# Kernel optimization log

Measured on AMD Instinct MI355X. Metric: run time of the kernel, lower is better.

Reference implementation:

```python
import jax, jax.numpy as jnp
import numpy as np

EMB_DIM, NUM_LEVELS, NUM_HEADS, NUM_POINTS = 256, 4, 8, 4
LEVEL_SHAPES = np.array([[128, 128], [64, 64], [32, 32], [16, 16]], dtype=np.int64)
B, N_Q = 8, 900
N_IMG = int((LEVEL_SHAPES[:, 0] * LEVEL_SHAPES[:, 1]).sum())  # 21760


def _offset_bias():
    # Faithful to the torch init: per-head square pattern scaled by point index.
    H, L, P = NUM_HEADS, NUM_LEVELS, NUM_POINTS
    angles = jnp.linspace(0.0, 2.0 * np.pi * (H - 1) / H, H)
    circle = jnp.stack([jnp.sin(angles), jnp.cos(angles)], axis=-1)          # [H,2]
    square = circle / jnp.max(jnp.abs(circle), axis=-1, keepdims=True)       # [H,2]
    squares = jnp.tile(square[:, None, None, :], (1, L, P, 1))               # [H,L,P,2]
    squares = squares * jnp.arange(1, P + 1, dtype=jnp.float32)[:, None]
    return squares.reshape(-1).astype(jnp.float32)


def setup_inputs() -> dict:
    key = jax.random.key(0)
    ks = jax.random.split(key, 12)
    C = EMB_DIM
    H, L, P = NUM_HEADS, NUM_LEVELS, NUM_POINTS
    s = 0.02
    return {
        'query_feat': jax.random.normal(ks[0], (B, N_Q, C), jnp.float32),
        'query_points': jax.random.uniform(ks[1], (B, N_Q, 4), jnp.float32, 0.1, 0.9),
        'img_feat': jax.random.normal(ks[2], (B, N_IMG, C), jnp.float32),
        'img_valid_ratios': jnp.ones((B, L, 2), jnp.float32),
        'img_mask': jnp.zeros((B, N_IMG), bool),
        'img_shapes': jnp.asarray(LEVEL_SHAPES),
        'W_img': jax.random.normal(ks[3], (C, C), jnp.float32) * s,
        'b_img': jax.random.normal(ks[4], (C,), jnp.float32) * s,
        'W_off': jax.random.normal(ks[5], (C, H * L * P * 2), jnp.float32) * 0.001,
        'b_off': _offset_bias(),
        'W_attn': jax.random.normal(ks[6], (C, H * L * P), jnp.float32) * s,
        'b_attn': jax.random.normal(ks[7], (H * L * P,), jnp.float32) * s,
        'W_out': jax.random.normal(ks[8], (C, C), jnp.float32) * s,
        'b_out': jax.random.normal(ks[9], (C,), jnp.float32) * s,
    }


def _bilinear_sample(value, loc, Hl, Wl):
    # value: [B,Hh,Hl*Wl,d]; loc: [B,Hh,Q,P,2] (x,y) normalized to [0,1]
    # grid_sample bilinear, padding_mode='zeros', align_corners=False
    Bb, Hh = value.shape[0], value.shape[1]
    x = loc[..., 0] * Wl - 0.5
    y = loc[..., 1] * Hl - 0.5
    x0f = jnp.floor(x); y0f = jnp.floor(y)
    wx = x - x0f; wy = y - y0f
    x0 = x0f.astype(jnp.int32); y0 = y0f.astype(jnp.int32)

    def gather(yi, xi):
        valid = (yi >= 0) & (yi < Hl) & (xi >= 0) & (xi < Wl)
        idx = jnp.clip(yi, 0, Hl - 1) * Wl + jnp.clip(xi, 0, Wl - 1)
        flat = idx.reshape(Bb, Hh, -1)[..., None]                 # [B,Hh,Q*P,1]
        g = jnp.take_along_axis(value, flat, axis=2)              # [B,Hh,Q*P,d]
        g = g.reshape(*idx.shape, value.shape[-1])                # [B,Hh,Q,P,d]
        return g * valid[..., None]

    v00 = gather(y0, x0); v01 = gather(y0, x0 + 1)
    v10 = gather(y0 + 1, x0); v11 = gather(y0 + 1, x0 + 1)
    w00 = ((1 - wy) * (1 - wx))[..., None]; w01 = ((1 - wy) * wx)[..., None]
    w10 = (wy * (1 - wx))[..., None]; w11 = (wy * wx)[..., None]
    return v00 * w00 + v01 * w01 + v10 * w10 + v11 * w11


def _msda(img_feat, img_shapes, sampling_points, attention_weights):
    # img_feat [B,N,Hh,d]; sampling_points [B,Q,Hh,L,P,2]; attn [B,Q,Hh,L,P]
    shapes = np.asarray(img_shapes)  # static level metadata
    Bb, N, Hh, d = img_feat.shape
    Q = sampling_points.shape[1]
    value = jnp.transpose(img_feat, (0, 2, 1, 3))                     # [B,Hh,N,d]
    loc = jnp.transpose(sampling_points, (0, 2, 1, 3, 4, 5))          # [B,Hh,Q,L,P,2]
    attn = jnp.transpose(attention_weights, (0, 2, 1, 3, 4))          # [B,Hh,Q,L,P]
    out = jnp.zeros((Bb, Hh, Q, d), img_feat.dtype)
    start = 0
    for l in range(shapes.shape[0]):
        Hl, Wl = int(shapes[l, 0]), int(shapes[l, 1])
        v = value[:, :, start:start + Hl * Wl]
        s = _bilinear_sample(v, loc[:, :, :, l], Hl, Wl)              # [B,Hh,Q,P,d]
        out = out + jnp.einsum('bhqpd,bhqp->bhqd', s, attn[:, :, :, l])
        start += Hl * Wl
    return jnp.transpose(out, (0, 2, 1, 3)).reshape(Bb, Q, Hh * d)


def reference(query_feat, query_points, img_feat, img_valid_ratios, img_mask,
              img_shapes, W_img, b_img, W_off, b_off, W_attn, b_attn, W_out, b_out):
    Bb, N_img, C = img_feat.shape
    N_q = query_feat.shape[1]
    Hh, L, P = NUM_HEADS, NUM_LEVELS, NUM_POINTS
    v = img_feat @ W_img + b_img
    v = jnp.where(img_mask[..., None], 0.0, v).reshape(Bb, N_img, Hh, C // Hh)
    offs = (query_feat @ W_off + b_off).reshape(Bb, N_q, Hh, L, P, 2)
    attn = jax.nn.softmax((query_feat @ W_attn + b_attn).reshape(Bb, N_q, Hh, L * P), axis=-1)
    attn = attn.reshape(Bb, N_q, Hh, L, P)
    # box branch (query_points last dim == 4), cxcywh relative coords
    vr = jnp.tile(img_valid_ratios[..., ::-1], (1, 1, 2))             # [B,L,4]
    qp = query_points[:, :, None, :] * vr[:, None, :, :]              # [B,Nq,L,4]
    sp = qp[:, :, None, :, None, :2] + offs * qp[:, :, None, :, None, 2:] / (2.0 * P)
    out = _msda(v, img_shapes, sp, attn)                              # [B,Nq,C]
    return out @ W_out + b_out
```

## Files before the change

kernel.cpp:

```cpp
#include <hip/hip_runtime.h>

#define NQ 900
#define NIMG 21760

typedef __attribute__((ext_vector_type(8))) short short8v;
typedef __attribute__((ext_vector_type(4))) float f32x4;
typedef unsigned short ushort_t;

__device__ __forceinline__ ushort_t f32_to_bf16_rne(float a) {
  unsigned u = __float_as_uint(a);
  unsigned r = u + 0x7FFFu + ((u >> 16) & 1u);
  return (ushort_t)(r >> 16);
}

union U8v {
  unsigned u[4];
  short8v v;
};

__device__ __forceinline__ short8v cvt8(float4 x, float4 y) {
  U8v r;
  asm("v_cvt_pk_bf16_f32 %0, %1, %2" : "=v"(r.u[0]) : "v"(x.x), "v"(x.y));
  asm("v_cvt_pk_bf16_f32 %0, %1, %2" : "=v"(r.u[1]) : "v"(x.z), "v"(x.w));
  asm("v_cvt_pk_bf16_f32 %0, %1, %2" : "=v"(r.u[2]) : "v"(y.x), "v"(y.y));
  asm("v_cvt_pk_bf16_f32 %0, %1, %2" : "=v"(r.u[3]) : "v"(y.z), "v"(y.w));
  return r.v;
}

__device__ __forceinline__ unsigned cvt_pk2(float a, float b) {
  unsigned r;
  asm("v_cvt_pk_bf16_f32 %0, %1, %2" : "=v"(r) : "v"(a), "v"(b));
  return r;
}

__global__ __launch_bounds__(256) void wprep_kernel(
    const float* __restrict__ Wimg, const float* __restrict__ Wout,
    ushort_t* __restrict__ Wh, ushort_t* __restrict__ Wh2) {
  const int blk = blockIdx.x;
  const int idx = (blk & 255) * 256 + threadIdx.x;
  const int k = idx >> 8, col = idx & 255;
  if (blk < 256)
    Wh[col * 256 + k] = f32_to_bf16_rne(Wimg[idx]);
  else
    Wh2[col * 256 + k] = f32_to_bf16_rne(Wout[idx]);
}

#define NBLK 512
#define NTILES 5440
__global__ __launch_bounds__(256, 2) void vproj_persist(
    const float* __restrict__ A, const ushort_t* __restrict__ Wh,
    const float* __restrict__ bias, ushort_t* __restrict__ v) {
  __shared__ __align__(16) float Abuf[2][32 * 256];

  const int t = threadIdx.x;
  const int w = t >> 6, lane = t & 63;
  const int lr = lane & 15, lg = lane >> 4;

  short8v bB[8][4];
#pragma unroll
  for (int ks = 0; ks < 8; ++ks)
#pragma unroll
    for (int n = 0; n < 4; ++n) {
      const int col = w * 64 + n * 16 + lr;
      bB[ks][n] = *(const short8v*)(Wh + (size_t)col * 256 + ks * 32 + lg * 8);
    }
  float bj[4][4];
#pragma unroll
  for (int n = 0; n < 4; ++n)
#pragma unroll
    for (int j = 0; j < 4; ++j) bj[n][j] = bias[w * 64 + n * 16 + lg * 4 + j];

  auto STAGE = [&](int buf, int tile) {
#pragma unroll
    for (int j = 0; j < 8; ++j) {
      const int ob = j * 4096 + w * 1024;
      const int o = ob + lane * 16;
      const int r = o >> 10;
      const int ir = (o & 1023) ^ ((r & 7) << 4);
      const float* gp = A + (size_t)(tile * 32 + r) * 256 + (ir >> 2);
      char* lp = (char*)(&Abuf[buf][0]) + ob;
      __builtin_amdgcn_global_load_lds(
          (const __attribute__((address_space(1))) void*)gp,
          (__attribute__((address_space(3))) void*)lp, 16, 0, 0);
    }
  };

  int tile = blockIdx.x;
  STAGE(0, tile);
  int cur = 0;

  for (; tile < NTILES; tile += NBLK) {
    const int nxt = tile + NBLK;
    if (nxt < NTILES) {
      STAGE(cur ^ 1, nxt);
      if (tile == (int)blockIdx.x)
        asm volatile("s_waitcnt vmcnt(8)" ::: "memory");
      else
        asm volatile("s_waitcnt vmcnt(16)" ::: "memory");
    } else {
      asm volatile("s_waitcnt vmcnt(8)" ::: "memory");
    }
    __builtin_amdgcn_s_barrier();
    __builtin_amdgcn_sched_barrier(0);

    f32x4 acc[2][4];
#pragma unroll
    for (int m = 0; m < 2; ++m)
#pragma unroll
      for (int n = 0; n < 4; ++n) {
        acc[m][n][0] = 0.f; acc[m][n][1] = 0.f;
        acc[m][n][2] = 0.f; acc[m][n][3] = 0.f;
      }

    const char* AB = (const char*)&Abuf[cur][0];

    float4 px[2][2], py[2][2];
#pragma unroll
    for (int p = 0; p < 2; ++p)
#pragma unroll
      for (int m = 0; m < 2; ++m) {
        const int row = m * 16 + lr;
        const int a0 = row * 1024 + ((p * 128 + lg * 32) ^ ((row & 7) << 4));
        px[p][m] = *(const float4*)(AB + a0);
        py[p][m] = *(const float4*)(AB + (a0 ^ 16));
      }

#pragma unroll
    for (int ks = 0; ks < 8; ++ks) {
      short8v ah[2];
#pragma unroll
      for (int m = 0; m < 2; ++m) ah[m] = cvt8(px[ks & 1][m], py[ks & 1][m]);
      if (ks < 6) {
#pragma unroll
        for (int m = 0; m < 2; ++m) {
          const int row = m * 16 + lr;
          const int a0 =
              row * 1024 + (((ks + 2) * 128 + lg * 32) ^ ((row & 7) << 4));
          px[ks & 1][m] = *(const float4*)(AB + a0);
          py[ks & 1][m] = *(const float4*)(AB + (a0 ^ 16));
        }
      }
#pragma unroll
      for (int n = 0; n < 4; ++n)
#pragma unroll
        for (int m = 0; m < 2; ++m)
          acc[m][n] = __builtin_amdgcn_mfma_f32_16x16x32_bf16(bB[ks][n], ah[m], acc[m][n], 0, 0, 0);
    }
    __builtin_amdgcn_sched_barrier(0);

    const int bb = tile / 680;
    const int pix0 = (tile - bb * 680) * 32;
#pragma unroll
    for (int n = 0; n < 4; ++n) {
      const int col0 = w * 64 + n * 16 + lg * 4;
      const int h = col0 >> 5, ch = col0 & 31;
#pragma unroll
      for (int m = 0; m < 2; ++m) {
        const int pixel = pix0 + m * 16 + lr;
        uint2 pk;
        pk.x = cvt_pk2(acc[m][n][0] + bj[n][0], acc[m][n][1] + bj[n][1]);
        pk.y = cvt_pk2(acc[m][n][2] + bj[n][2], acc[m][n][3] + bj[n][3]);
        *(uint2*)(v + ((size_t)(bb * 8 + h) * NIMG + pixel) * 32 + ch) = pk;
      }
    }
    __builtin_amdgcn_s_barrier();
    cur ^= 1;
  }
}

__global__ __launch_bounds__(256) void gemm_noLds(
    const float* __restrict__ A, const ushort_t* __restrict__ Wh,
    const float* __restrict__ bias, float* __restrict__ C, int M) {
  const int t = threadIdx.x;
  const int colblk = blockIdx.x & 3;
  const int rowblk = blockIdx.x >> 2;
  const int col0 = colblk * 64;

  const int lane = t & 63, w = t >> 6;
  const int lr = lane & 15, lg = lane >> 4;
  const int wrow0 = rowblk * 64 + w * 16;

  f32x4 acc[4];
#pragma unroll
  for (int n = 0; n < 4; ++n) {
    acc[n][0] = 0.f; acc[n][1] = 0.f; acc[n][2] = 0.f; acc[n][3] = 0.f;
  }

#pragma unroll
  for (int ks = 0; ks < 8; ++ks) {
    int row = wrow0 + lr;
    row = min(row, M - 1);
    const float4* ap = (const float4*)(A + (size_t)row * 256 + ks * 32 + lg * 8);
    const short8v ah = cvt8(ap[0], ap[1]);
    const int k0 = ks * 32 + lg * 8;
#pragma unroll
    for (int n = 0; n < 4; ++n) {
      const int col = col0 + n * 16 + lr;
      const short8v bh = *(const short8v*)(Wh + col * 256 + k0);
      acc[n] = __builtin_amdgcn_mfma_f32_16x16x32_bf16(ah, bh, acc[n], 0, 0, 0);
    }
  }

#pragma unroll
  for (int n = 0; n < 4; ++n) {
    const int col = col0 + n * 16 + lr;
    const float b = bias[col];
#pragma unroll
    for (int j = 0; j < 4; ++j) {
      const int row = wrow0 + lg * 4 + j;
      if (row < M) C[(size_t)row * 256 + col] = acc[n][j] + b;
    }
  }
}

__global__ __launch_bounds__(384) void qproj_kernel(
    const float* __restrict__ qf, const float* __restrict__ qpts_g,
    const float* __restrict__ ivr, const float* __restrict__ Woff,
    const float* __restrict__ boff, const float* __restrict__ Wattn,
    const float* __restrict__ battn, float* __restrict__ sp,
    float* __restrict__ attn) {
  __shared__ __align__(16) float qlds[8 * 256];
  __shared__ float qp[8][4];
  __shared__ float vr[8][8];
  __shared__ float logits[8][128];
  const int t = threadIdx.x;
  const int row0 = blockIdx.x * 8;

  for (int idx = t; idx < 8 * 256; idx += 384)
    qlds[idx] = qf[(size_t)row0 * 256 + idx];
  if (t < 32) {
    const int m = t >> 2, j = t & 3;
    qp[m][j] = qpts_g[(size_t)(row0 + m) * 4 + j];
  }
  if (t >= 32 && t < 96) {
    const int u = t - 32;
    const int m = u >> 3, j = u & 7;
    const int b = (row0 + m) / NQ;
    vr[m][j] = ivr[b * 8 + j];
  }
  __syncthreads();

  float acc[8];
#pragma unroll
  for (int m = 0; m < 8; ++m) acc[m] = 0.f;

  const float4* q4 = (const float4*)qlds;
  const int c = t - 256;
  for (int k4 = 0; k4 < 64; ++k4) {
    float w0, w1, w2, w3;
    if (t < 256) {
      w0 = Woff[(k4 * 4 + 0) * 256 + t];
      w1 = Woff[(k4 * 4 + 1) * 256 + t];
      w2 = Woff[(k4 * 4 + 2) * 256 + t];
      w3 = Woff[(k4 * 4 + 3) * 256 + t];
    } else {
      w0 = Wattn[(k4 * 4 + 0) * 128 + c];
      w1 = Wattn[(k4 * 4 + 1) * 128 + c];
      w2 = Wattn[(k4 * 4 + 2) * 128 + c];
      w3 = Wattn[(k4 * 4 + 3) * 128 + c];
    }
#pragma unroll
    for (int m = 0; m < 8; ++m) {
      const float4 f = q4[m * 64 + k4];
      acc[m] = fmaf(f.x, w0, acc[m]);
      acc[m] = fmaf(f.y, w1, acc[m]);
      acc[m] = fmaf(f.z, w2, acc[m]);
      acc[m] = fmaf(f.w, w3, acc[m]);
    }
  }

  if (t >= 256) {
    const float bb = battn[c];
#pragma unroll
    for (int m = 0; m < 8; ++m) logits[m][c] = acc[m] + bb;
  }
  __syncthreads();

  if (t < 64) {
    const int m = t >> 3, h = t & 7;
    float mx = -1e30f;
#pragma unroll
    for (int j = 0; j < 16; ++j) mx = fmaxf(mx, logits[m][h * 16 + j]);
    float e[16];
    float s = 0.f;
#pragma unroll
    for (int j = 0; j < 16; ++j) {
      e[j] = expf(logits[m][h * 16 + j] - mx);
      s += e[j];
    }
    const float inv = 1.f / s;
    const size_t row = row0 + m;
#pragma unroll
    for (int j = 0; j < 16; ++j) attn[row * 128 + h * 16 + j] = e[j] * inv;
  }

  if (t < 256) {
    const int xy = t & 1;
    const int l = (t >> 3) & 3;
    const float bo = boff[t];
#pragma unroll
    for (int m = 0; m < 8; ++m) {
      const float val = acc[m] + bo;
      const float r = vr[m][l * 2 + (xy ^ 1)];
      const float ctr = qp[m][xy] * r;
      const float scl = qp[m][2 + xy] * r * 0.125f;
      sp[(size_t)(row0 + m) * 256 + t] = ctr + val * scl;
    }
  }
}

__global__ __launch_bounds__(256) void msda_kernel(
    const ushort_t* __restrict__ v, const float* __restrict__ sp,
    const float* __restrict__ attn, float* __restrict__ outk) {
  __shared__ __align__(16) float splds[1024];
  __shared__ __align__(16) float alds[512];
  __shared__ int ioff[16 * 2 * 32];
  __shared__ float wgt[16 * 4 * 32];
  const int t = threadIdx.x;
  const int bid = (int)(blockIdx.x & 7) * 225 + (int)(blockIdx.x >> 3);
  const int row0 = bid * 4;

  ((float4*)splds)[t] = ((const float4*)(sp + (size_t)row0 * 256))[t];
  if (t < 128)
    ((float4*)alds)[t] = ((const float4*)(attn + (size_t)row0 * 128))[t];
  __syncthreads();

#pragma unroll
  for (int it = 0; it < 2; ++it) {
    const int s = it * 256 + t;
    const int q = s >> 7, h = (s >> 4) & 7, l = (s >> 2) & 3, p = s & 3;
    const int un = q * 8 + h;
    const int j = l * 4 + p;
    const float spx = splds[q * 256 + h * 32 + l * 8 + p * 2];
    const float spy = splds[q * 256 + h * 32 + l * 8 + p * 2 + 1];
    const float a = alds[q * 128 + h * 16 + l * 4 + p];
    const int WL = 128 >> l;
    const int start = (65536 - (65536 >> (2 * l))) / 3;
    const float x = spx * (float)WL - 0.5f;
    const float y = spy * (float)WL - 0.5f;
    const float x0f = floorf(x), y0f = floorf(y);
    const float wx = x - x0f, wy = y - y0f;
    const int x0 = (int)x0f, y0 = (int)y0f;
    const int x1 = x0 + 1, y1 = y0 + 1;
    const int bx = min(max(x0, 0), WL - 2);
    const bool vx0 = (x0 >= 0) & (x0 < WL), vx1 = (x1 >= 0) & (x1 < WL);
    float wxl = 0.f, wxr = 0.f;
    if (vx0 & (x0 == bx)) wxl += 1.f - wx;
    if (vx1 & (x1 == bx)) wxl += wx;
    if (vx0 & (x0 == bx + 1)) wxr += 1.f - wx;
    if (vx1 & (x1 == bx + 1)) wxr += wx;
    const int cy0 = min(max(y0, 0), WL - 1), cy1 = min(max(y1, 0), WL - 1);
    const float ay0 = ((y0 >= 0) & (y0 < WL)) ? a * (1.f - wy) : 0.f;
    const float ay1 = ((y1 >= 0) & (y1 < WL)) ? a * wy : 0.f;
    ioff[(j * 2 + 0) * 32 + un] = (start + cy0 * WL + bx) * 32;
    ioff[(j * 2 + 1) * 32 + un] = (start + cy1 * WL + bx) * 32;
    wgt[(j * 4 + 0) * 32 + un] = ay0 * wxl;
    wgt[(j * 4 + 1) * 32 + un] = ay0 * wxr;
    wgt[(j * 4 + 2) * 32 + un] = ay1 * wxl;
    wgt[(j * 4 + 3) * 32 + un] = ay1 * wxr;
  }
  __syncthreads();

  const int q = t >> 6, h = (t >> 3) & 7, d8 = t & 7;
  const int un = q * 8 + h;
  const int cq = d8 & 3, half = d8 >> 2;
  const int row = row0 + q;
  const int b = row / NQ;
  const ushort_t* vbl =
      v + ((size_t)(b * 8 + h) * NIMG) * 32 + half * 32 + cq * 8;

  float acc[8];
#pragma unroll
  for (int i = 0; i < 8; ++i) acc[i] = 0.f;

#pragma unroll
  for (int j = 0; j < 16; ++j) {
#pragma unroll
    for (int r = 0; r < 2; ++r) {
      const int off = ioff[(j * 2 + r) * 32 + un];
      const float wc = wgt[(j * 4 + r * 2 + half) * 32 + un];
      const uint4 uu = *(const uint4*)(vbl + off);
      acc[0] = fmaf(wc, __uint_as_float(uu.x << 16), acc[0]);
      acc[1] = fmaf(wc, __uint_as_float(uu.x & 0xFFFF0000u), acc[1]);
      acc[2] = fmaf(wc, __uint_as_float(uu.y << 16), acc[2]);
      acc[3] = fmaf(wc, __uint_as_float(uu.y & 0xFFFF0000u), acc[3]);
      acc[4] = fmaf(wc, __uint_as_float(uu.z << 16), acc[4]);
      acc[5] = fmaf(wc, __uint_as_float(uu.z & 0xFFFF0000u), acc[5]);
      acc[6] = fmaf(wc, __uint_as_float(uu.w << 16), acc[6]);
      acc[7] = fmaf(wc, __uint_as_float(uu.w & 0xFFFF0000u), acc[7]);
    }
  }

#pragma unroll
  for (int i = 0; i < 8; ++i) acc[i] += __shfl_xor(acc[i], 4);

  float4 o;
  o.x = acc[half * 4 + 0];
  o.y = acc[half * 4 + 1];
  o.z = acc[half * 4 + 2];
  o.w = acc[half * 4 + 3];
  *(float4*)(outk + (size_t)row * 256 + h * 32 + cq * 8 + half * 4) = o;
}

extern "C" void kernel_launch(void* const* d_in, const int* in_sizes, int n_in,
                              void* d_out, int out_size, void* d_ws, size_t ws_size,
                              hipStream_t stream) {
  const float* query_feat   = (const float*)d_in[0];
  const float* query_points = (const float*)d_in[1];
  const float* img_feat     = (const float*)d_in[2];
  const float* ivr          = (const float*)d_in[3];
  const float* W_img  = (const float*)d_in[6];
  const float* b_img  = (const float*)d_in[7];
  const float* W_off  = (const float*)d_in[8];
  const float* b_off  = (const float*)d_in[9];
  const float* W_attn = (const float*)d_in[10];
  const float* b_attn = (const float*)d_in[11];
  const float* W_out  = (const float*)d_in[12];
  const float* b_out  = (const float*)d_in[13];
  float* out = (float*)d_out;

  float* ws   = (float*)d_ws;
  ushort_t* v = (ushort_t*)ws;
  float* sp   = (float*)(v + 44564480);
  float* attn = sp + 1843200;
  float* mso  = attn + 921600;
  ushort_t* Wh  = (ushort_t*)(mso + 1843200);
  ushort_t* Wh2 = Wh + 65536;

  wprep_kernel<<<512, 256, 0, stream>>>(W_img, W_out, Wh, Wh2);
  vproj_persist<<<NBLK, 256, 0, stream>>>(img_feat, Wh, b_img, v);
  qproj_kernel<<<900, 384, 0, stream>>>(query_feat, query_points, ivr,
                                        W_off, b_off, W_attn, b_attn, sp, attn);
  msda_kernel<<<1800, 256, 0, stream>>>(v, sp, attn, mso);
  gemm_noLds<<<113 * 4, 256, 0, stream>>>(mso, Wh2, b_out, out, 7200);
}
```

Before: 141.3 us.

## Remap MSDA blocks to one head per block and double query rows in qproj

The sampling kernel now gives each block 32 queries of a single (batch, head) pair instead of 4 queries across all 8 heads. Every block therefore gathers from one head's value slab, which should improve cache locality for the bilinear gathers. Sampling points and attention weights are read straight from global memory rather than staged in shared memory, and a guarded tail handles query counts that are not a multiple of 32. Separately, the query projection processes 16 rows per block so each weight load is reused twice as often, at the cost of more registers and fewer blocks.

```diff
diff --git a/kernel.cpp b/kernel.cpp
--- a/kernel.cpp
+++ b/kernel.cpp
@@ -219,30 +219,30 @@
     const float* __restrict__ boff, const float* __restrict__ Wattn,
     const float* __restrict__ battn, float* __restrict__ sp,
     float* __restrict__ attn) {
-  __shared__ __align__(16) float qlds[8 * 256];
-  __shared__ float qp[8][4];
-  __shared__ float vr[8][8];
-  __shared__ float logits[8][128];
+  __shared__ __align__(16) float qlds[16 * 256];
+  __shared__ float qp[16][4];
+  __shared__ float vr[16][8];
+  __shared__ float logits[16][128];
   const int t = threadIdx.x;
-  const int row0 = blockIdx.x * 8;
-
-  for (int idx = t; idx < 8 * 256; idx += 384)
+  const int row0 = blockIdx.x * 16;
+
+  for (int idx = t; idx < 16 * 256; idx += 384)
     qlds[idx] = qf[(size_t)row0 * 256 + idx];
-  if (t < 32) {
+  if (t < 64) {
     const int m = t >> 2, j = t & 3;
     qp[m][j] = qpts_g[(size_t)(row0 + m) * 4 + j];
   }
-  if (t >= 32 && t < 96) {
-    const int u = t - 32;
+  if (t >= 64 && t < 192) {
+    const int u = t - 64;
     const int m = u >> 3, j = u & 7;
     const int b = (row0 + m) / NQ;
     vr[m][j] = ivr[b * 8 + j];
   }
   __syncthreads();
 
-  float acc[8];
-#pragma unroll
-  for (int m = 0; m < 8; ++m) acc[m] = 0.f;
+  float acc[16];
+#pragma unroll
+  for (int m = 0; m < 16; ++m) acc[m] = 0.f;
 
   const float4* q4 = (const float4*)qlds;
   const int c = t - 256;
@@ -260,7 +260,7 @@
       w3 = Wattn[(k4 * 4 + 3) * 128 + c];
     }
 #pragma unroll
-    for (int m = 0; m < 8; ++m) {
+    for (int m = 0; m < 16; ++m) {
       const float4 f = q4[m * 64 + k4];
       acc[m] = fmaf(f.x, w0, acc[m]);
       acc[m] = fmaf(f.y, w1, acc[m]);
@@ -272,11 +272,11 @@
   if (t >= 256) {
     const float bb = battn[c];
 #pragma unroll
-    for (int m = 0; m < 8; ++m) logits[m][c] = acc[m] + bb;
+    for (int m = 0; m < 16; ++m) logits[m][c] = acc[m] + bb;
   }
   __syncthreads();
 
-  if (t < 64) {
+  if (t < 128) {
     const int m = t >> 3, h = t & 7;
     float mx = -1e30f;
 #pragma unroll
@@ -299,7 +299,7 @@
     const int l = (t >> 3) & 3;
     const float bo = boff[t];
 #pragma unroll
-    for (int m = 0; m < 8; ++m) {
+    for (int m = 0; m < 16; ++m) {
       const float val = acc[m] + bo;
       const float r = vr[m][l * 2 + (xy ^ 1)];
       const float ctr = qp[m][xy] * r;
@@ -309,31 +309,28 @@
   }
 }
 
+#define QCH 29
 __global__ __launch_bounds__(256) void msda_kernel(
     const ushort_t* __restrict__ v, const float* __restrict__ sp,
     const float* __restrict__ attn, float* __restrict__ outk) {
-  __shared__ __align__(16) float splds[1024];
-  __shared__ __align__(16) float alds[512];
   __shared__ int ioff[16 * 2 * 32];
   __shared__ float wgt[16 * 4 * 32];
   const int t = threadIdx.x;
-  const int bid = (int)(blockIdx.x & 7) * 225 + (int)(blockIdx.x >> 3);
-  const int row0 = bid * 4;
-
-  ((float4*)splds)[t] = ((const float4*)(sp + (size_t)row0 * 256))[t];
-  if (t < 128)
-    ((float4*)alds)[t] = ((const float4*)(attn + (size_t)row0 * 128))[t];
-  __syncthreads();
+  const int b = blockIdx.x & 7;
+  const int inner = blockIdx.x >> 3;
+  const int h = inner / QCH;
+  const int q0 = (inner - h * QCH) * 32;
 
 #pragma unroll
   for (int it = 0; it < 2; ++it) {
     const int s = it * 256 + t;
-    const int q = s >> 7, h = (s >> 4) & 7, l = (s >> 2) & 3, p = s & 3;
-    const int un = q * 8 + h;
-    const int j = l * 4 + p;
-    const float spx = splds[q * 256 + h * 32 + l * 8 + p * 2];
-    const float spy = splds[q * 256 + h * 32 + l * 8 + p * 2 + 1];
-    const float a = alds[q * 128 + h * 16 + l * 4 + p];
+    const int ql = s >> 4, j = s & 15;
+    const int l = j >> 2, p = j & 3;
+    const bool valid = (q0 + ql) < NQ;
+    const size_t row = (size_t)b * NQ + (valid ? q0 + ql : 0);
+    const float spx = valid ? sp[row * 256 + h * 32 + l * 8 + p * 2] : 0.5f;
+    const float spy = valid ? sp[row * 256 + h * 32 + l * 8 + p * 2 + 1] : 0.5f;
+    const float a = valid ? attn[row * 128 + h * 16 + j] : 0.f;
     const int WL = 128 >> l;
     const int start = (65536 - (65536 >> (2 * l))) / 3;
     const float x = spx * (float)WL - 0.5f;
@@ -352,20 +349,17 @@
     const int cy0 = min(max(y0, 0), WL - 1), cy1 = min(max(y1, 0), WL - 1);
     const float ay0 = ((y0 >= 0) & (y0 < WL)) ? a * (1.f - wy) : 0.f;
     const float ay1 = ((y1 >= 0) & (y1 < WL)) ? a * wy : 0.f;
-    ioff[(j * 2 + 0) * 32 + un] = (start + cy0 * WL + bx) * 32;
-    ioff[(j * 2 + 1) * 32 + un] = (start + cy1 * WL + bx) * 32;
-    wgt[(j * 4 + 0) * 32 + un] = ay0 * wxl;
-    wgt[(j * 4 + 1) * 32 + un] = ay0 * wxr;
-    wgt[(j * 4 + 2) * 32 + un] = ay1 * wxl;
-    wgt[(j * 4 + 3) * 32 + un] = ay1 * wxr;
+    ioff[(j * 2 + 0) * 32 + ql] = (start + cy0 * WL + bx) * 32;
+    ioff[(j * 2 + 1) * 32 + ql] = (start + cy1 * WL + bx) * 32;
+    wgt[(j * 4 + 0) * 32 + ql] = ay0 * wxl;
+    wgt[(j * 4 + 1) * 32 + ql] = ay0 * wxr;
+    wgt[(j * 4 + 2) * 32 + ql] = ay1 * wxl;
+    wgt[(j * 4 + 3) * 32 + ql] = ay1 * wxr;
   }
   __syncthreads();
 
-  const int q = t >> 6, h = (t >> 3) & 7, d8 = t & 7;
-  const int un = q * 8 + h;
+  const int ql = t >> 3, d8 = t & 7;
   const int cq = d8 & 3, half = d8 >> 2;
-  const int row = row0 + q;
-  const int b = row / NQ;
   const ushort_t* vbl =
       v + ((size_t)(b * 8 + h) * NIMG) * 32 + half * 32 + cq * 8;
 
@@ -377,8 +371,8 @@
   for (int j = 0; j < 16; ++j) {
 #pragma unroll
     for (int r = 0; r < 2; ++r) {
-      const int off = ioff[(j * 2 + r) * 32 + un];
-      const float wc = wgt[(j * 4 + r * 2 + half) * 32 + un];
+      const int off = ioff[(j * 2 + r) * 32 + ql];
+      const float wc = wgt[(j * 4 + r * 2 + half) * 32 + ql];
       const uint4 uu = *(const uint4*)(vbl + off);
       acc[0] = fmaf(wc, __uint_as_float(uu.x << 16), acc[0]);
       acc[1] = fmaf(wc, __uint_as_float(uu.x & 0xFFFF0000u), acc[1]);
@@ -394,12 +388,15 @@
 #pragma unroll
   for (int i = 0; i < 8; ++i) acc[i] += __shfl_xor(acc[i], 4);
 
-  float4 o;
-  o.x = acc[half * 4 + 0];
-  o.y = acc[half * 4 + 1];
-  o.z = acc[half * 4 + 2];
-  o.w = acc[half * 4 + 3];
-  *(float4*)(outk + (size_t)row * 256 + h * 32 + cq * 8 + half * 4) = o;
+  if (q0 + ql < NQ) {
+    const size_t row = (size_t)b * NQ + q0 + ql;
+    float4 o;
+    o.x = acc[half * 4 + 0];
+    o.y = acc[half * 4 + 1];
+    o.z = acc[half * 4 + 2];
+    o.w = acc[half * 4 + 3];
+    *(float4*)(outk + row * 256 + h * 32 + cq * 8 + half * 4) = o;
+  }
 }
 
 extern "C" void kernel_launch(void* const* d_in, const int* in_sizes, int n_in,
@@ -429,8 +426,8 @@
 
   wprep_kernel<<<512, 256, 0, stream>>>(W_img, W_out, Wh, Wh2);
   vproj_persist<<<NBLK, 256, 0, stream>>>(img_feat, Wh, b_img, v);
-  qproj_kernel<<<900, 384, 0, stream>>>(query_feat, query_points, ivr,
+  qproj_kernel<<<450, 384, 0, stream>>>(query_feat, query_points, ivr,
                                         W_off, b_off, W_attn, b_attn, sp, attn);
-  msda_kernel<<<1800, 256, 0, stream>>>(v, sp, attn, mso);
+  msda_kernel<<<8 * 8 * QCH, 256, 0, stream>>>(v, sp, attn, mso);
   gemm_noLds<<<113 * 4, 256, 0, stream>>>(mso, Wh2, b_out, out, 7200);
 }
```

Measured after the change: 152.3 us. +7.8%, slower.

## Fuse query projection into value-projection kernel as extra blocks

Applied to the files above, without the earlier changes.

Merges the query offset/attention projection kernel into the persistent value-projection kernel, dispatching 900 query blocks first and 512 value-projection blocks after in one launch. The two independent projections can then overlap on the GPU, and one launch gap goes away. The query path is remapped from 384 to 256 threads: threads 128-255 compute both offset and attention columns, and the shared-memory scratch is reused from the staging buffer. Risks are register pressure from the combined kernel under launch_bounds(256,2), and the persistent value blocks starting late behind the query blocks.

```diff
diff --git a/kernel.cpp b/kernel.cpp
--- a/kernel.cpp
+++ b/kernel.cpp
@@ -45,14 +45,115 @@
     Wh2[col * 256 + k] = f32_to_bf16_rne(Wout[idx]);
 }
 
-#define NBLK 512
+#define QBLKS 900
+#define VBLKS 512
 #define NTILES 5440
-__global__ __launch_bounds__(256, 2) void vproj_persist(
+__global__ __launch_bounds__(256, 2) void fused_vq(
     const float* __restrict__ A, const ushort_t* __restrict__ Wh,
-    const float* __restrict__ bias, ushort_t* __restrict__ v) {
+    const float* __restrict__ bias, ushort_t* __restrict__ v,
+    const float* __restrict__ qf, const float* __restrict__ qpts_g,
+    const float* __restrict__ ivr, const float* __restrict__ Woff,
+    const float* __restrict__ boff, const float* __restrict__ Wattn,
+    const float* __restrict__ battn, float* __restrict__ sp,
+    float* __restrict__ attn) {
   __shared__ __align__(16) float Abuf[2][32 * 256];
 
   const int t = threadIdx.x;
+
+  if (blockIdx.x < QBLKS) {
+    float* qlds = &Abuf[0][0];
+    float* qp = qlds + 2048;
+    float* vr = qp + 32;
+    float* logits = vr + 64;
+    const int row0 = blockIdx.x * 8;
+
+#pragma unroll
+    for (int i = 0; i < 8; ++i) qlds[i * 256 + t] = qf[(size_t)row0 * 256 + i * 256 + t];
+    if (t < 32) qp[t] = qpts_g[(size_t)row0 * 4 + t];
+    if (t >= 32 && t < 96) {
+      const int u = t - 32;
+      const int m = u >> 3, j = u & 7;
+      const int b = (row0 + m) / NQ;
+      vr[m * 8 + j] = ivr[b * 8 + j];
+    }
+    __syncthreads();
+
+    float acc[8], acc2[8];
+#pragma unroll
+    for (int m = 0; m < 8; ++m) { acc[m] = 0.f; acc2[m] = 0.f; }
+
+    const float4* q4 = (const float4*)qlds;
+    const int c = t - 128;
+    for (int k4 = 0; k4 < 64; ++k4) {
+      const float w0 = Woff[(k4 * 4 + 0) * 256 + t];
+      const float w1 = Woff[(k4 * 4 + 1) * 256 + t];
+      const float w2 = Woff[(k4 * 4 + 2) * 256 + t];
+      const float w3 = Woff[(k4 * 4 + 3) * 256 + t];
+      float a0 = 0.f, a1 = 0.f, a2 = 0.f, a3 = 0.f;
+      if (t >= 128) {
+        a0 = Wattn[(k4 * 4 + 0) * 128 + c];
+        a1 = Wattn[(k4 * 4 + 1) * 128 + c];
+        a2 = Wattn[(k4 * 4 + 2) * 128 + c];
+        a3 = Wattn[(k4 * 4 + 3) * 128 + c];
+      }
+#pragma unroll
+      for (int m = 0; m < 8; ++m) {
+        const float4 f = q4[m * 64 + k4];
+        acc[m] = fmaf(f.x, w0, acc[m]);
+        acc[m] = fmaf(f.y, w1, acc[m]);
+        acc[m] = fmaf(f.z, w2, acc[m]);
+        acc[m] = fmaf(f.w, w3, acc[m]);
+        if (t >= 128) {
+          acc2[m] = fmaf(f.x, a0, acc2[m]);
+          acc2[m] = fmaf(f.y, a1, acc2[m]);
+          acc2[m] = fmaf(f.z, a2, acc2[m]);
+          acc2[m] = fmaf(f.w, a3, acc2[m]);
+        }
+      }
+    }
+
+    if (t >= 128) {
+      const float bb = battn[c];
+#pragma unroll
+      for (int m = 0; m < 8; ++m) logits[m * 128 + c] = acc2[m] + bb;
+    }
+    __syncthreads();
+
+    if (t < 64) {
+      const int m = t >> 3, h = t & 7;
+      float mx = -1e30f;
+#pragma unroll
+      for (int j = 0; j < 16; ++j) mx = fmaxf(mx, logits[m * 128 + h * 16 + j]);
+      float e[16];
+      float s = 0.f;
+#pragma unroll
+      for (int j = 0; j < 16; ++j) {
+        e[j] = expf(logits[m * 128 + h * 16 + j] - mx);
+        s += e[j];
+      }
+      const float inv = 1.f / s;
+      const size_t row = row0 + m;
+#pragma unroll
+      for (int j = 0; j < 16; ++j) attn[row * 128 + h * 16 + j] = e[j] * inv;
+    }
+
+    {
+      const int xy = t & 1;
+      const int l = (t >> 3) & 3;
+      const float bo = boff[t];
+#pragma unroll
+      for (int m = 0; m < 8; ++m) {
+        const float val = acc[m] + bo;
+        const float r = vr[m * 8 + l * 2 + (xy ^ 1)];
+        const float ctr = qp[m * 4 + xy] * r;
+        const float scl = qp[m * 4 + 2 + xy] * r * 0.125f;
+        sp[(size_t)(row0 + m) * 256 + t] = ctr + val * scl;
+      }
+    }
+    return;
+  }
+
+  const int vbid = blockIdx.x - QBLKS;
   const int w = t >> 6, lane = t & 63;
   const int lr = lane & 15, lg = lane >> 4;
 
@@ -85,15 +186,15 @@
     }
   };
 
-  int tile = blockIdx.x;
+  int tile = vbid;
   STAGE(0, tile);
   int cur = 0;
 
-  for (; tile < NTILES; tile += NBLK) {
-    const int nxt = tile + NBLK;
+  for (; tile < NTILES; tile += VBLKS) {
+    const int nxt = tile + VBLKS;
     if (nxt < NTILES) {
       STAGE(cur ^ 1, nxt);
-      if (tile == (int)blockIdx.x)
+      if (tile == vbid)
         asm volatile("s_waitcnt vmcnt(8)" ::: "memory");
       else
         asm volatile("s_waitcnt vmcnt(16)" ::: "memory");
@@ -209,102 +310,6 @@
     for (int j = 0; j < 4; ++j) {
       const int row = wrow0 + lg * 4 + j;
       if (row < M) C[(size_t)row * 256 + col] = acc[n][j] + b;
-    }
-  }
-}
-
-__global__ __launch_bounds__(384) void qproj_kernel(
-    const float* __restrict__ qf, const float* __restrict__ qpts_g,
-    const float* __restrict__ ivr, const float* __restrict__ Woff,
-    const float* __restrict__ boff, const float* __restrict__ Wattn,
-    const float* __restrict__ battn, float* __restrict__ sp,
-    float* __restrict__ attn) {
-  __shared__ __align__(16) float qlds[8 * 256];
-  __shared__ float qp[8][4];
-  __shared__ float vr[8][8];
-  __shared__ float logits[8][128];
-  const int t = threadIdx.x;
-  const int row0 = blockIdx.x * 8;
-
-  for (int idx = t; idx < 8 * 256; idx += 384)
-    qlds[idx] = qf[(size_t)row0 * 256 + idx];
-  if (t < 32) {
-    const int m = t >> 2, j = t & 3;
-    qp[m][j] = qpts_g[(size_t)(row0 + m) * 4 + j];
-  }
-  if (t >= 32 && t < 96) {
-    const int u = t - 32;
-    const int m = u >> 3, j = u & 7;
-    const int b = (row0 + m) / NQ;
-    vr[m][j] = ivr[b * 8 + j];
-  }
-  __syncthreads();
-
-  float acc[8];
-#pragma unroll
-  for (int m = 0; m < 8; ++m) acc[m] = 0.f;
-
-  const float4* q4 = (const float4*)qlds;
-  const int c = t - 256;
-  for (int k4 = 0; k4 < 64; ++k4) {
-    float w0, w1, w2, w3;
-    if (t < 256) {
-      w0 = Woff[(k4 * 4 + 0) * 256 + t];
-      w1 = Woff[(k4 * 4 + 1) * 256 + t];
-      w2 = Woff[(k4 * 4 + 2) * 256 + t];
-      w3 = Woff[(k4 * 4 + 3) * 256 + t];
-    } else {
-      w0 = Wattn[(k4 * 4 + 0) * 128 + c];
-      w1 = Wattn[(k4 * 4 + 1) * 128 + c];
-      w2 = Wattn[(k4 * 4 + 2) * 128 + c];
-      w3 = Wattn[(k4 * 4 + 3) * 128 + c];
-    }
-#pragma unroll
-    for (int m = 0; m < 8; ++m) {
-      const float4 f = q4[m * 64 + k4];
-      acc[m] = fmaf(f.x, w0, acc[m]);
-      acc[m] = fmaf(f.y, w1, acc[m]);
-      acc[m] = fmaf(f.z, w2, acc[m]);
-      acc[m] = fmaf(f.w, w3, acc[m]);
-    }
-  }
-
-  if (t >= 256) {
-    const float bb = battn[c];
-#pragma unroll
-    for (int m = 0; m < 8; ++m) logits[m][c] = acc[m] + bb;
-  }
-  __syncthreads();
-
-  if (t < 64) {
-    const int m = t >> 3, h = t & 7;
-    float mx = -1e30f;
-#pragma unroll
-    for (int j = 0; j < 16; ++j) mx = fmaxf(mx, logits[m][h * 16 + j]);
-    float e[16];
-    float s = 0.f;
-#pragma unroll
-    for (int j = 0; j < 16; ++j) {
-      e[j] = expf(logits[m][h * 16 + j] - mx);
-      s += e[j];
-    }
-    const float inv = 1.f / s;
-    const size_t row = row0 + m;
-#pragma unroll
-    for (int j = 0; j < 16; ++j) attn[row * 128 + h * 16 + j] = e[j] * inv;
-  }
-
-  if (t < 256) {
-    const int xy = t & 1;
-    const int l = (t >> 3) & 3;
-    const float bo = boff[t];
-#pragma unroll
-    for (int m = 0; m < 8; ++m) {
-      const float val = acc[m] + bo;
-      const float r = vr[m][l * 2 + (xy ^ 1)];
-      const float ctr = qp[m][xy] * r;
-      const float scl = qp[m][2 + xy] * r * 0.125f;
-      sp[(size_t)(row0 + m) * 256 + t] = ctr + val * scl;
     }
   }
 }
@@ -428,9 +433,9 @@
   ushort_t* Wh2 = Wh + 65536;
 
   wprep_kernel<<<512, 256, 0, stream>>>(W_img, W_out, Wh, Wh2);
-  vproj_persist<<<NBLK, 256, 0, stream>>>(img_feat, Wh, b_img, v);
-  qproj_kernel<<<900, 384, 0, stream>>>(query_feat, query_points, ivr,
-                                        W_off, b_off, W_attn, b_attn, sp, attn);
+  fused_vq<<<QBLKS + VBLKS, 256, 0, stream>>>(
+      img_feat, Wh, b_img, v, query_feat, query_points, ivr, W_off, b_off,
+      W_attn, b_attn, sp, attn);
   msda_kernel<<<1800, 256, 0, stream>>>(v, sp, attn, mso);
   gemm_noLds<<<113 * 4, 256, 0, stream>>>(mso, Wh2, b_out, out, 7200);
 }
```

Result: slower. 159.4 us (+12.8%).

## Use 16-row tiles with a 4-stage async LDS pipeline in vproj

Applied to the files above, without the earlier changes.

The persistent value-projection GEMM now processes 16-row tiles instead of 32-row tiles and keeps four LDS buffers in flight instead of two. It stages three tiles ahead and uses hand-tuned vmcnt waits for each pipeline phase. The aim is to hide more global-load latency for the memory-bound fp32 input stream. The cost is half the MFMA work per barrier pair and more tile iterations with their barrier overhead.

```diff
diff --git a/kernel.cpp b/kernel.cpp
--- a/kernel.cpp
+++ b/kernel.cpp
@@ -46,15 +46,16 @@
 }
 
 #define NBLK 512
-#define NTILES 5440
+#define NT16 10880
 __global__ __launch_bounds__(256, 2) void vproj_persist(
     const float* __restrict__ A, const ushort_t* __restrict__ Wh,
     const float* __restrict__ bias, ushort_t* __restrict__ v) {
-  __shared__ __align__(16) float Abuf[2][32 * 256];
+  __shared__ __align__(16) float Abuf[4][16 * 256];
 
   const int t = threadIdx.x;
   const int w = t >> 6, lane = t & 63;
   const int lr = lane & 15, lg = lane >> 4;
+  const int bid = blockIdx.x;
 
   short8v bB[8][4];
 #pragma unroll
@@ -70,14 +71,16 @@
 #pragma unroll
     for (int j = 0; j < 4; ++j) bj[n][j] = bias[w * 64 + n * 16 + lg * 4 + j];
 
-  auto STAGE = [&](int buf, int tile) {
-#pragma unroll
-    for (int j = 0; j < 8; ++j) {
+  auto STAGE = [&](int k) {
+    const int buf = k & 3;
+    const float* base = A + (size_t)(bid + (size_t)k * NBLK) * (16 * 256);
+#pragma unroll
+    for (int j = 0; j < 4; ++j) {
       const int ob = j * 4096 + w * 1024;
       const int o = ob + lane * 16;
       const int r = o >> 10;
       const int ir = (o & 1023) ^ ((r & 7) << 4);
-      const float* gp = A + (size_t)(tile * 32 + r) * 256 + (ir >> 2);
+      const float* gp = base + r * 256 + (ir >> 2);
       char* lp = (char*)(&Abuf[buf][0]) + ob;
       __builtin_amdgcn_global_load_lds(
           (const __attribute__((address_space(1))) void*)gp,
@@ -85,86 +88,67 @@
     }
   };
 
-  int tile = blockIdx.x;
-  STAGE(0, tile);
-  int cur = 0;
-
-  for (; tile < NTILES; tile += NBLK) {
-    const int nxt = tile + NBLK;
-    if (nxt < NTILES) {
-      STAGE(cur ^ 1, nxt);
-      if (tile == (int)blockIdx.x)
-        asm volatile("s_waitcnt vmcnt(8)" ::: "memory");
-      else
-        asm volatile("s_waitcnt vmcnt(16)" ::: "memory");
-    } else {
-      asm volatile("s_waitcnt vmcnt(8)" ::: "memory");
-    }
+  const int nt = (NT16 - bid + NBLK - 1) / NBLK;
+  STAGE(0);
+  STAGE(1);
+  STAGE(2);
+
+  for (int k = 0; k < nt; ++k) {
+    if (k + 3 < nt) STAGE(k + 3);
+    if (k == 0)           asm volatile("s_waitcnt vmcnt(12)" ::: "memory");
+    else if (k == 1)      asm volatile("s_waitcnt vmcnt(16)" ::: "memory");
+    else if (k == 2)      asm volatile("s_waitcnt vmcnt(20)" ::: "memory");
+    else if (k + 3 < nt)  asm volatile("s_waitcnt vmcnt(24)" ::: "memory");
+    else if (k + 2 < nt)  asm volatile("s_waitcnt vmcnt(20)" ::: "memory");
+    else if (k + 1 < nt)  asm volatile("s_waitcnt vmcnt(16)" ::: "memory");
+    else                  asm volatile("s_waitcnt vmcnt(12)" ::: "memory");
     __builtin_amdgcn_s_barrier();
     __builtin_amdgcn_sched_barrier(0);
 
-    f32x4 acc[2][4];
-#pragma unroll
-    for (int m = 0; m < 2; ++m)
-#pragma unroll
-      for (int n = 0; n < 4; ++n) {
-        acc[m][n][0] = 0.f; acc[m][n][1] = 0.f;
-        acc[m][n][2] = 0.f; acc[m][n][3] = 0.f;
+    f32x4 acc[4];
+#pragma unroll
+    for (int n = 0; n < 4; ++n) {
+      acc[n][0] = 0.f; acc[n][1] = 0.f; acc[n][2] = 0.f; acc[n][3] = 0.f;
+    }
+
+    const char* AB = (const char*)&Abuf[k & 3][0];
+
+    float4 px[2], py[2];
+#pragma unroll
+    for (int p = 0; p < 2; ++p) {
+      const int a0 = lr * 1024 + ((p * 128 + lg * 32) ^ ((lr & 7) << 4));
+      px[p] = *(const float4*)(AB + a0);
+      py[p] = *(const float4*)(AB + (a0 ^ 16));
+    }
+
+#pragma unroll
+    for (int ks = 0; ks < 8; ++ks) {
+      const short8v ah = cvt8(px[ks & 1], py[ks & 1]);
+      if (ks < 6) {
+        const int a0 = lr * 1024 + (((ks + 2) * 128 + lg * 32) ^ ((lr & 7) << 4));
+        px[ks & 1] = *(const float4*)(AB + a0);
+        py[ks & 1] = *(const float4*)(AB + (a0 ^ 16));
       }
-
-    const char* AB = (const char*)&Abuf[cur][0];
-
-    float4 px[2][2], py[2][2];
-#pragma unroll
-    for (int p = 0; p < 2; ++p)
-#pragma unroll
-      for (int m = 0; m < 2; ++m) {
-        const int row = m * 16 + lr;
-        const int a0 = row * 1024 + ((p * 128 + lg * 32) ^ ((row & 7) << 4));
-        px[p][m] = *(const float4*)(AB + a0);
-        py[p][m] = *(const float4*)(AB + (a0 ^ 16));
-      }
-
-#pragma unroll
-    for (int ks = 0; ks < 8; ++ks) {
-      short8v ah[2];
-#pragma unroll
-      for (int m = 0; m < 2; ++m) ah[m] = cvt8(px[ks & 1][m], py[ks & 1][m]);
-      if (ks < 6) {
-#pragma unroll
-        for (int m = 0; m < 2; ++m) {
-          const int row = m * 16 + lr;
-          const int a0 =
-              row * 1024 + (((ks + 2) * 128 + lg * 32) ^ ((row & 7) << 4));
-          px[ks & 1][m] = *(const float4*)(AB + a0);
-          py[ks & 1][m] = *(const float4*)(AB + (a0 ^ 16));
-        }
-      }
 #pragma unroll
       for (int n = 0; n < 4; ++n)
-#pragma unroll
-        for (int m = 0; m < 2; ++m)
-          acc[m][n] = __builtin_amdgcn_mfma_f32_16x16x32_bf16(bB[ks][n], ah[m], acc[m][n], 0, 0, 0);
+        acc[n] = __builtin_amdgcn_mfma_f32_16x16x32_bf16(bB[ks][n], ah, acc[n], 0, 0, 0);
     }
     __builtin_amdgcn_sched_barrier(0);
 
-    const int bb = tile / 680;
-    const int pix0 = (tile - bb * 680) * 32;
+    const int tile = bid + k * NBLK;
+    const int bb = tile / 1360;
+    const int pix0 = (tile - bb * 1360) * 16;
+    const int pixel = pix0 + lr;
 #pragma unroll
     for (int n = 0; n < 4; ++n) {
       const int col0 = w * 64 + n * 16 + lg * 4;
       const int h = col0 >> 5, ch = col0 & 31;
-#pragma unroll
-      for (int m = 0; m < 2; ++m) {
-        const int pixel = pix0 + m * 16 + lr;
-        uint2 pk;
-        pk.x = cvt_pk2(acc[m][n][0] + bj[n][0], acc[m][n][1] + bj[n][1]);
-        pk.y = cvt_pk2(acc[m][n][2] + bj[n][2], acc[m][n][3] + bj[n][3]);
-        *(uint2*)(v + ((size_t)(bb * 8 + h) * NIMG + pixel) * 32 + ch) = pk;
-      }
+      uint2 pk;
+      pk.x = cvt_pk2(acc[n][0] + bj[n][0], acc[n][1] + bj[n][1]);
+      pk.y = cvt_pk2(acc[n][2] + bj[n][2], acc[n][3] + bj[n][3]);
+      *(uint2*)(v + ((size_t)(bb * 8 + h) * NIMG + pixel) * 32 + ch) = pk;
     }
     __builtin_amdgcn_s_barrier();
-    cur ^= 1;
   }
 }
 
```

Measured after the change: 140.2 us, median of 2. About the same (-0.8%).
